# Kernel optimization log

Measured on AMD Instinct MI355X. Metric: run time of the kernel, lower is better.

## Reference

```python
import jax, jax.numpy as jnp
import numpy as np

HID, INP, BATCH, TIME = 1024, 512, 128, 256


def _kaiming(key, d1, d2, gain):
    # kaiming_normal_: std = gain / sqrt(fan_in), fan_in = d2
    return jax.random.normal(key, (d1, d2), jnp.float32) * (gain / np.sqrt(d2))


def setup_inputs() -> dict:
    key = jax.random.key(0)
    ks = jax.random.split(key, 9)
    g_lin = 1.0          # nonlinearity='linear'
    g_tanh = 5.0 / 3.0   # nonlinearity='tanh'
    inp = {
        "x": jax.random.normal(ks[0], (BATCH, TIME, INP), jnp.float32),
        "c": jnp.zeros((HID, BATCH), jnp.float32),
        "h": jnp.zeros((HID, BATCH), jnp.float32),
        "W_gx": _kaiming(ks[1], HID, INP, g_lin),
        "W_ix": _kaiming(ks[2], HID, INP, g_lin),
        "W_fx": _kaiming(ks[3], HID, INP, g_lin),
        "W_ox": _kaiming(ks[4], HID, INP, g_lin),
        "W_gh": _kaiming(ks[5], HID, HID, g_tanh),
        "W_ih": _kaiming(ks[6], HID, HID, g_tanh),
        "W_fh": _kaiming(ks[7], HID, HID, g_tanh),
        "W_oh": _kaiming(ks[8], HID, HID, g_tanh),
        "b_g": jnp.zeros((HID, 1), jnp.float32),
        "b_i": jnp.zeros((HID, 1), jnp.float32),
        "b_f": jnp.zeros((HID, 1), jnp.float32),
        "b_o": jnp.zeros((HID, 1), jnp.float32),
    }
    return inp


def reference(x, c, h, W_gx, W_ix, W_fx, W_ox, W_gh, W_ih, W_fh, W_oh,
              b_g, b_i, b_f, b_o):
    Hd = W_gx.shape[0]
    # Fuse the four gate GEMMs into one: same math, single contraction.
    Wx = jnp.concatenate([W_gx, W_ix, W_fx, W_ox], axis=0)   # (4H, I)
    Wh = jnp.concatenate([W_gh, W_ih, W_fh, W_oh], axis=0)   # (4H, H)
    b = jnp.concatenate([b_g, b_i, b_f, b_o], axis=0)[:, 0]  # (4H,)
    # Precompute all input projections: (T, B, 4H)
    xs = jnp.einsum('bti,gi->tbg', x, Wx)

    def step(carry, xt):
        c_t, h_t = carry                      # (B, H)
        z = xt + h_t @ Wh.T + b               # (B, 4H)
        g = jnp.tanh(z[:, :Hd])
        i = jax.nn.sigmoid(z[:, Hd:2 * Hd])
        f = jax.nn.sigmoid(z[:, 2 * Hd:3 * Hd])
        o = jax.nn.sigmoid(z[:, 3 * Hd:])
        c_n = g * i + c_t * f
        h_n = jnp.tanh(c_n) * o
        return (c_n, h_n), None

    (c_f, h_f), _ = jax.lax.scan(step, (c.T, h.T), xs)
    return h_f.T  # (H, B), matching the torch layout
```

## Files before the change

### kernel.cpp

```cpp
#include <hip/hip_runtime.h>
#include <cstdint>
#include <cstddef>

#define HID 1024
#define INP 512
#define BATCH 128
#define TSTEPS 256
#define NK16 96
#define ZSLOTS 32

using short8  = __attribute__((ext_vector_type(8))) short;
using f32x16  = __attribute__((ext_vector_type(16))) float;

#define LD8(p) (*(const short8*)(p))
#define MFMA32(a,b,c) __builtin_amdgcn_mfma_f32_32x32x16_bf16((a),(b),(c),0,0,0)

static __device__ __forceinline__ unsigned short f2bf(float f) {
    union { float f; unsigned int u; } v; v.f = f;
    unsigned int r = v.u + 0x7fffu + ((v.u >> 16) & 1u);
    return (unsigned short)(r >> 16);
}
static __device__ __forceinline__ float bf2f(unsigned short b) {
    union { unsigned int u; float f; } v; v.u = ((unsigned int)b) << 16;
    return v.f;
}
static __device__ __forceinline__ float sigmoid_f(float z) {
    return 1.0f / (1.0f + __expf(-z));
}
static __device__ __forceinline__ float tanh_f(float z) {
    return 2.0f / (1.0f + __expf(-2.0f * z)) - 1.0f;
}


__global__ void prep_w(const float* __restrict__ Wgx, const float* __restrict__ Wix,
                       const float* __restrict__ Wfx, const float* __restrict__ Wox,
                       const float* __restrict__ Wgh, const float* __restrict__ Wih,
                       const float* __restrict__ Wfh, const float* __restrict__ Woh,
                       unsigned short* __restrict__ wfrag)
{
    const int k16 = blockIdx.x;
    const int s   = blockIdx.y;
    const int tid  = threadIdx.x;
    const int lane = tid >> 2;
    const int e0   = (tid & 3) * 2;
    const int row  = s * 32 + (lane & 31);
    const int k    = k16 * 16 + (lane >> 5) * 8 + e0;
    const int j = row >> 2;
    const int g = row & 3;
    float f0, f1;
    if (k < INP) {
        const float* wx = (g == 0 ? Wgx : g == 1 ? Wix : g == 2 ? Wfx : Wox) + (size_t)j * INP;
        f0 = wx[k]; f1 = wx[k + 1];
    } else {
        const float* wh = (g == 0 ? Wgh : g == 1 ? Wih : g == 2 ? Wfh : Woh) + (size_t)j * HID;
        f0 = wh[k - INP]; f1 = wh[k - INP + 1];
    }
    ushort2 hi, lo;
    hi.x = f2bf(f0); lo.x = f2bf(f0 - bf2f(hi.x));
    hi.y = f2bf(f1); lo.y = f2bf(f1 - bf2f(hi.y));
    unsigned short* base = wfrag + ((size_t)(s * NK16 + k16) * 2) * 512 + lane * 8 + e0;
    *(ushort2*)(base)       = hi;
    *(ushort2*)(base + 512) = lo;
}

__global__ void prep_x(const float* __restrict__ x, unsigned short* __restrict__ xfrag)
{
    const int k16x = blockIdx.x;
    const int t    = blockIdx.y;
    const int tid  = threadIdx.x;
    const int cg   = tid >> 6;
    const int lane = tid & 63;
    const int col  = cg * 32 + (lane & 31);
    const int k0   = k16x * 16 + (lane >> 5) * 8;
    const float* src = x + ((size_t)col * TSTEPS + t) * INP + k0;
    const float4 v0 = *(const float4*)(src);
    const float4 v1 = *(const float4*)(src + 4);
    ushort4 h0, l0, h1, l1;
    h0.x = f2bf(v0.x); l0.x = f2bf(v0.x - bf2f(h0.x));
    h0.y = f2bf(v0.y); l0.y = f2bf(v0.y - bf2f(h0.y));
    h0.z = f2bf(v0.z); l0.z = f2bf(v0.z - bf2f(h0.z));
    h0.w = f2bf(v0.w); l0.w = f2bf(v0.w - bf2f(h0.w));
    h1.x = f2bf(v1.x); l1.x = f2bf(v1.x - bf2f(h1.x));
    h1.y = f2bf(v1.y); l1.y = f2bf(v1.y - bf2f(h1.y));
    h1.z = f2bf(v1.z); l1.z = f2bf(v1.z - bf2f(h1.z));
    h1.w = f2bf(v1.w); l1.w = f2bf(v1.w - bf2f(h1.w));
    unsigned short* base = xfrag +
        ((size_t)(((size_t)t * 32 + k16x) * 4 + cg) * 2) * 512 + lane * 8;
    *(ushort4*)(base)           = h0;
    *(ushort4*)(base + 4)       = h1;
    *(ushort4*)(base + 512)     = l0;
    *(ushort4*)(base + 512 + 4) = l1;
}

__global__ void prep_state(const float* __restrict__ cin, const float* __restrict__ hin,
                           float* __restrict__ cdst, unsigned short* __restrict__ hfrag0)
{
    const int idx = blockIdx.x * 256 + threadIdx.x;
    cdst[idx] = cin[idx];
    const int j = idx >> 7;
    const int b = idx & 127;
    float f = hin[idx];
    unsigned short hh = f2bf(f);
    unsigned short hl = f2bf(f - bf2f(hh));
    const int k16h = j >> 4;
    const int hlf  = (j >> 3) & 1;
    const int e    = j & 7;
    const int cg   = b >> 5;
    const int lane = 32 * hlf + (b & 31);
    unsigned short* base = hfrag0 +
        ((size_t)((k16h * 4 + cg) * 2) * 512) + lane * 8 + e;
    base[0]   = hh;
    base[512] = hl;
}

__global__ __launch_bounds__(512, 2) void gemm_z0(
    const unsigned short* __restrict__ wfrag,
    const unsigned short* __restrict__ xfrag,
    float* __restrict__ z0,
    const float* __restrict__ bg, const float* __restrict__ bi,
    const float* __restrict__ bf_, const float* __restrict__ bo,
    int tbase)
{
    const int tid  = threadIdx.x;
    const int wv   = tid >> 6;
    const int lane = tid & 63;
    const int l31  = lane & 31;
    const int hl   = lane >> 5;
    const int cw   = wv & 1;
    const int kq   = wv >> 1;
    const int s    = blockIdx.x;
    const int t    = tbase + blockIdx.y;
    const int tslot = t & (ZSLOTS - 1);

    const unsigned short* pA = wfrag + ((size_t)(s * NK16 + kq) * 2) * 512 + lane * 8;
    const unsigned short* pB = xfrag + (size_t)t * 131072
                             + (size_t)(4 * kq + 2 * cw) * 1024 + lane * 8;

    f32x16 a0A, a0B, a1A, a1B;
#pragma unroll
    for (int r = 0; r < 16; ++r) { a0A[r]=0.f; a0B[r]=0.f; a1A[r]=0.f; a1B[r]=0.f; }

#pragma unroll
    for (int m = 0; m < 8; ++m) {
        short8 Ah  = LD8(pA);
        short8 Al  = LD8(pA + 512);
        short8 B0h = LD8(pB);
        short8 B0l = LD8(pB + 512);
        short8 B1h = LD8(pB + 1024);
        short8 B1l = LD8(pB + 1536);
        pA += 4096; pB += 16384;
        a0A = MFMA32(Ah, B0h, a0A);
        a1A = MFMA32(Ah, B1h, a1A);
        a0B = MFMA32(Ah, B0l, a0B);
        a1B = MFMA32(Ah, B1l, a1B);
        a0A = MFMA32(Al, B0h, a0A);
        a1A = MFMA32(Al, B1h, a1A);
    }

    __shared__ float part[2][32][128];

    if (kq >= 2) {
#pragma unroll
        for (int r = 0; r < 16; ++r) {
            const int lr = (r & 3) + 8 * (r >> 2) + 4 * hl;
            part[kq - 2][lr][(2 * cw)     * 32 + l31] = a0A[r] + a0B[r];
            part[kq - 2][lr][(2 * cw + 1) * 32 + l31] = a1A[r] + a1B[r];
        }
    }
    __syncthreads();
    if (kq < 2) {
#pragma unroll
        for (int r = 0; r < 16; ++r) {
            const int lr = (r & 3) + 8 * (r >> 2) + 4 * hl;
            part[kq][lr][(2 * cw)     * 32 + l31] += a0A[r] + a0B[r];
            part[kq][lr][(2 * cw + 1) * 32 + l31] += a1A[r] + a1B[r];
        }
    }
    __syncthreads();

    {
        const int lr = tid >> 4;
        const int c0 = (tid & 15) * 8;
        const int g  = lr & 3;
        const int j  = s * 8 + (lr >> 2);
        const float bb = (g == 0 ? bg : g == 1 ? bi : g == 2 ? bf_ : bo)[j];
        float z[8];
#pragma unroll
        for (int cc = 0; cc < 8; ++cc)
            z[cc] = part[0][lr][c0 + cc] + part[1][lr][c0 + cc] + bb;
        float* dst = z0 + (((size_t)tslot * 128 + s) * 32 + lr) * 128 + c0;
        *(float4*)(dst)     = make_float4(z[0], z[1], z[2], z[3]);
        *(float4*)(dst + 4) = make_float4(z[4], z[5], z[6], z[7]);
    }
}

__global__ __launch_bounds__(512, 1) void lstm_step(
    const unsigned short* __restrict__ wfrag,
    const unsigned short* __restrict__ xfrag,
    const float* __restrict__ z0,
    const unsigned short* __restrict__ hin,
    unsigned short* __restrict__ hout,
    float* __restrict__ cst,
    const float* __restrict__ bg, const float* __restrict__ bi,
    const float* __restrict__ bf_, const float* __restrict__ bo,
    float* __restrict__ outf, int t)
{
    const int tid  = threadIdx.x;
    const int wv   = tid >> 6;
    const int lane = tid & 63;
    const int l31  = lane & 31;
    const int hl   = lane >> 5;
    const int bx   = blockIdx.x;

    const int xcd     = bx & 7;
    const int ii      = bx >> 3;
    const int s       = xcd * 16 + (ii >> 1);
    const int cb      = ii & 1;
    const int colbase = cb << 6;
    const int J0      = s * 8;

    const int ejl  = tid >> 6;
    const int ecl  = tid & 63;
    const int ej   = J0 + ejl;
    const int ecol = colbase + ecl;

    float add0, add1, add2, add3;
    if (z0) {
        const float* zp = z0 + (((size_t)(t & (ZSLOTS - 1)) * 128 + s) * 32
                                + 4 * ejl) * 128 + ecol;
        add0 = zp[0]; add1 = zp[128]; add2 = zp[256]; add3 = zp[384];
    } else {
        add0 = bg[ej]; add1 = bi[ej]; add2 = bf_[ej]; add3 = bo[ej];
    }
    const size_t ci = (size_t)ej * BATCH + ecol;
    float cold = cst[ci];

    f32x16 a0A, a0B, a1A, a1B;
#pragma unroll
    for (int r = 0; r < 16; ++r) { a0A[r]=0.f; a0B[r]=0.f; a1A[r]=0.f; a1B[r]=0.f; }

    const size_t bOff = (size_t)(4 * wv + 2 * cb) * 1024 + lane * 8;

    if (z0) {
        const unsigned short* pA = wfrag + ((size_t)(s * NK16 + 32 + wv) * 2) * 512 + lane * 8;
        const unsigned short* pH = hin + bOff;
#pragma unroll
        for (int m = 0; m < 8; ++m) {
            short8 Ah  = LD8(pA);
            short8 Al  = LD8(pA + 512);
            short8 B0h = LD8(pH);
            short8 B0l = LD8(pH + 512);
            short8 B1h = LD8(pH + 1024);
            short8 B1l = LD8(pH + 1536);
            pA += 8192; pH += 32768;
            a0A = MFMA32(Ah, B0h, a0A);
            a1A = MFMA32(Ah, B1h, a1A);
            a0B = MFMA32(Ah, B0l, a0B);
            a1B = MFMA32(Ah, B1l, a1B);
            a0A = MFMA32(Al, B0h, a0A);
            a1A = MFMA32(Al, B1h, a1A);
        }
    } else {
        const unsigned short* pA = wfrag + ((size_t)(s * NK16 + wv) * 2) * 512 + lane * 8;
        const unsigned short* pX = xfrag + (size_t)t * 131072 + bOff;
#pragma unroll
        for (int m = 0; m < 4; ++m) {
            short8 Ah  = LD8(pA);
            short8 Al  = LD8(pA + 512);
            short8 B0h = LD8(pX);
            short8 B0l = LD8(pX + 512);
            short8 B1h = LD8(pX + 1024);
            short8 B1l = LD8(pX + 1536);
            pA += 8192; pX += 32768;
            a0A = MFMA32(Ah, B0h, a0A);
            a1A = MFMA32(Ah, B1h, a1A);
            a0B = MFMA32(Ah, B0l, a0B);
            a1B = MFMA32(Ah, B1l, a1B);
            a0A = MFMA32(Al, B0h, a0A);
            a1A = MFMA32(Al, B1h, a1A);
        }
        const unsigned short* pH = hin + bOff;
#pragma unroll
        for (int m = 0; m < 8; ++m) {
            short8 Ah  = LD8(pA);
            short8 Al  = LD8(pA + 512);
            short8 B0h = LD8(pH);
            short8 B0l = LD8(pH + 512);
            short8 B1h = LD8(pH + 1024);
            short8 B1l = LD8(pH + 1536);
            pA += 8192; pH += 32768;
            a0A = MFMA32(Ah, B0h, a0A);
            a1A = MFMA32(Ah, B1h, a1A);
            a0B = MFMA32(Ah, B0l, a0B);
            a1B = MFMA32(Ah, B1l, a1B);
            a0A = MFMA32(Al, B0h, a0A);
            a1A = MFMA32(Al, B1h, a1A);
        }
    }

    __shared__ float part[8][32][64];
#pragma unroll
    for (int r = 0; r < 16; ++r) {
        const int lr = (r & 3) + 8 * (r >> 2) + 4 * hl;
        part[wv][lr][l31]      = a0A[r] + a0B[r];
        part[wv][lr][32 + l31] = a1A[r] + a1B[r];
    }
    __syncthreads();

    {
        const int r0 = 4 * ejl;
        float z0g = add0, z1g = add1, z2g = add2, z3g = add3;
#pragma unroll
        for (int p = 0; p < 8; ++p) {
            z0g += part[p][r0 + 0][ecl];
            z1g += part[p][r0 + 1][ecl];
            z2g += part[p][r0 + 2][ecl];
            z3g += part[p][r0 + 3][ecl];
        }
        float gg = tanh_f(z0g);
        float ig = sigmoid_f(z1g);
        float fg = sigmoid_f(z2g);
        float og = sigmoid_f(z3g);
        float cn = gg * ig + cold * fg;
        cst[ci] = cn;
        float hh = tanh_f(cn) * og;
        unsigned short hb  = f2bf(hh);
        unsigned short hlo = f2bf(hh - bf2f(hb));
        const int k16h  = s >> 1;
        const int cgg   = (colbase >> 5) + (ecl >> 5);
        const int lane8 = 32 * (s & 1) + (ecl & 31);
        unsigned short* dst = hout +
            ((size_t)((k16h * 4 + cgg) * 2) * 512) + lane8 * 8 + ejl;
        dst[0]   = hb;
        dst[512] = hlo;
        if (outf) outf[ci] = hh;
    }
}

extern "C" void kernel_launch(void* const* d_in, const int* in_sizes, int n_in,
                              void* d_out, int out_size, void* d_ws, size_t ws_size,
                              hipStream_t stream)
{
    const float* x   = (const float*)d_in[0];
    const float* c0v = (const float*)d_in[1];
    const float* h0v = (const float*)d_in[2];
    const float* Wgx = (const float*)d_in[3];
    const float* Wix = (const float*)d_in[4];
    const float* Wfx = (const float*)d_in[5];
    const float* Wox = (const float*)d_in[6];
    const float* Wgh = (const float*)d_in[7];
    const float* Wih = (const float*)d_in[8];
    const float* Wfh = (const float*)d_in[9];
    const float* Woh = (const float*)d_in[10];
    const float* bg  = (const float*)d_in[11];
    const float* bi  = (const float*)d_in[12];
    const float* bf  = (const float*)d_in[13];
    const float* bo  = (const float*)d_in[14];

    unsigned short* wfrag = (unsigned short*)d_ws;
    unsigned short* xfrag = wfrag + (size_t)128 * NK16 * 2 * 512;
    unsigned short* hf0   = xfrag + (size_t)TSTEPS * 32 * 4 * 2 * 512;
    unsigned short* hf1   = hf0 + (size_t)64 * 4 * 2 * 512;
    float* cst            = (float*)(hf1 + (size_t)64 * 4 * 2 * 512);
    float* z0             = (float*)(cst + (size_t)HID * BATCH);

    const size_t needA = (size_t)((char*)(z0 + (size_t)ZSLOTS * 4096 * 128) - (char*)d_ws);
    const bool useA = (ws_size >= needA);

    unsigned short* hf[2] = { hf0, hf1 };
    float* outp = (float*)d_out;

    prep_w<<<dim3(NK16, 128), dim3(256), 0, stream>>>(Wgx, Wix, Wfx, Wox,
                                                      Wgh, Wih, Wfh, Woh, wfrag);
    prep_x<<<dim3(32, TSTEPS), dim3(256), 0, stream>>>(x, xfrag);
    prep_state<<<dim3(512), dim3(256), 0, stream>>>(c0v, h0v, cst, hf[0]);

    if (useA) {
        for (int q = 0; q < TSTEPS / ZSLOTS; ++q) {
            gemm_z0<<<dim3(128, ZSLOTS), dim3(512), 0, stream>>>(
                wfrag, xfrag, z0, bg, bi, bf, bo, q * ZSLOTS);
            for (int tt = 0; tt < ZSLOTS; ++tt) {
                const int t = q * ZSLOTS + tt;
                lstm_step<<<dim3(256), dim3(512), 0, stream>>>(
                    wfrag, xfrag, z0, hf[t & 1], hf[(t + 1) & 1],
                    cst, bg, bi, bf, bo,
                    (t == TSTEPS - 1) ? outp : nullptr, t);
            }
        }
    } else {
        for (int t = 0; t < TSTEPS; ++t) {
            lstm_step<<<dim3(256), dim3(512), 0, stream>>>(
                wfrag, xfrag, nullptr, hf[t & 1], hf[(t + 1) & 1],
                cst, bg, bi, bf, bo,
                (t == TSTEPS - 1) ? outp : nullptr, t);
        }
    }
}
```

Before: 2.514 ms.

## Replace per-step LSTM launches with a persistent cooperative kernel using flag barriers

Replaces the 256 per-timestep lstm_step launches and the batched input-projection GEMM with a single cooperative persistent kernel. Each block keeps its cell state in registers and computes both the x and h projections each step. Blocks synchronise through per-block atomic step flags in global memory, and h is written into a 32-slot ring buffer. This removes kernel launch overhead and the z0 round trip through memory. The cost is spin-wait polling on flags and a dependence on all 256 blocks being co-resident, which relies on relaxed atomics with an occasional acquire fence.

```diff
diff --git a/kernel.cpp b/kernel.cpp
--- a/kernel.cpp
+++ b/kernel.cpp
@@ -7,7 +7,9 @@
 #define BATCH 128
 #define TSTEPS 256
 #define NK16 96
-#define ZSLOTS 32
+#define HSLOTS 32
+#define NBLK_CHUNK 256
+#define HSLOT ((size_t)64 * 4 * 2 * 512)
 
 using short8  = __attribute__((ext_vector_type(8))) short;
 using f32x16  = __attribute__((ext_vector_type(16))) float;
@@ -93,8 +95,10 @@
 }
 
 __global__ void prep_state(const float* __restrict__ cin, const float* __restrict__ hin,
-                           float* __restrict__ cdst, unsigned short* __restrict__ hfrag0)
-{
+                           float* __restrict__ cdst, unsigned short* __restrict__ hslot,
+                           unsigned* __restrict__ flags)
+{
+    if (blockIdx.x == 0) flags[threadIdx.x] = 0u;
     const int idx = blockIdx.x * 256 + threadIdx.x;
     cdst[idx] = cin[idx];
     const int j = idx >> 7;
@@ -107,97 +111,178 @@
     const int e    = j & 7;
     const int cg   = b >> 5;
     const int lane = 32 * hlf + (b & 31);
-    unsigned short* base = hfrag0 +
+    unsigned short* base = hslot +
         ((size_t)((k16h * 4 + cg) * 2) * 512) + lane * 8 + e;
     base[0]   = hh;
     base[512] = hl;
 }
 
-__global__ __launch_bounds__(512, 2) void gemm_z0(
+__global__ __launch_bounds__(512, 1) void lstm_persist(
     const unsigned short* __restrict__ wfrag,
     const unsigned short* __restrict__ xfrag,
-    float* __restrict__ z0,
+    unsigned short* __restrict__ hbuf,
+    float* __restrict__ cst,
     const float* __restrict__ bg, const float* __restrict__ bi,
     const float* __restrict__ bf_, const float* __restrict__ bo,
-    int tbase)
+    float* __restrict__ outf,
+    unsigned* __restrict__ flags)
 {
     const int tid  = threadIdx.x;
     const int wv   = tid >> 6;
     const int lane = tid & 63;
     const int l31  = lane & 31;
     const int hl   = lane >> 5;
-    const int cw   = wv & 1;
-    const int kq   = wv >> 1;
-    const int s    = blockIdx.x;
-    const int t    = tbase + blockIdx.y;
-    const int tslot = t & (ZSLOTS - 1);
-
-    const unsigned short* pA = wfrag + ((size_t)(s * NK16 + kq) * 2) * 512 + lane * 8;
-    const unsigned short* pB = xfrag + (size_t)t * 131072
-                             + (size_t)(4 * kq + 2 * cw) * 1024 + lane * 8;
-
-    f32x16 a0A, a0B, a1A, a1B;
-#pragma unroll
-    for (int r = 0; r < 16; ++r) { a0A[r]=0.f; a0B[r]=0.f; a1A[r]=0.f; a1B[r]=0.f; }
-
-#pragma unroll
-    for (int m = 0; m < 8; ++m) {
-        short8 Ah  = LD8(pA);
-        short8 Al  = LD8(pA + 512);
-        short8 B0h = LD8(pB);
-        short8 B0l = LD8(pB + 512);
-        short8 B1h = LD8(pB + 1024);
-        short8 B1l = LD8(pB + 1536);
-        pA += 4096; pB += 16384;
-        a0A = MFMA32(Ah, B0h, a0A);
-        a1A = MFMA32(Ah, B1h, a1A);
-        a0B = MFMA32(Ah, B0l, a0B);
-        a1B = MFMA32(Ah, B1l, a1B);
-        a0A = MFMA32(Al, B0h, a0A);
-        a1A = MFMA32(Al, B1h, a1A);
-    }
-
-    __shared__ float part[2][32][128];
-
-    if (kq >= 2) {
+    const int bx   = blockIdx.x;
+
+    const int xcd     = bx & 7;
+    const int ii      = bx >> 3;
+    const int s       = xcd * 16 + (ii >> 1);
+    const int cb      = ii & 1;
+    const int colbase = cb << 6;
+
+    const int ejl  = tid >> 6;
+    const int ecl  = tid & 63;
+    const int ej   = s * 8 + ejl;
+    const int ecol = colbase + ecl;
+    const size_t ci = (size_t)ej * BATCH + ecol;
+
+    const float bias0 = bg[ej], bias1 = bi[ej], bias2 = bf_[ej], bias3 = bo[ej];
+    float creg = cst[ci];
+
+    const size_t bOff = (size_t)(4 * wv + 2 * cb) * 1024 + lane * 8;
+    const int k16h = s >> 1;
+
+    const unsigned short* pAx0 = wfrag + ((size_t)(s * NK16 + wv) * 2) * 512 + lane * 8;
+    const unsigned short* pAh0 = wfrag + ((size_t)(s * NK16 + 32 + wv) * 2) * 512 + lane * 8;
+
+    __shared__ float part[8][32][64];
+    __shared__ unsigned long long hstage[256];
+    unsigned short* hs16 = (unsigned short*)hstage;
+
+#pragma unroll 1
+    for (int t = 0; t < TSTEPS; ++t) {
+        f32x16 a0A, a0B, a1A, a1B;
+#pragma unroll
+        for (int r = 0; r < 16; ++r) { a0A[r]=0.f; a0B[r]=0.f; a1A[r]=0.f; a1B[r]=0.f; }
+
+        {
+            const unsigned short* pA = pAx0;
+            const unsigned short* pX = xfrag + (size_t)t * 131072 + bOff;
+#pragma unroll
+            for (int m = 0; m < 4; ++m) {
+                short8 Ah  = LD8(pA);
+                short8 Al  = LD8(pA + 512);
+                short8 B0h = LD8(pX);
+                short8 B0l = LD8(pX + 512);
+                short8 B1h = LD8(pX + 1024);
+                short8 B1l = LD8(pX + 1536);
+                pA += 8192; pX += 32768;
+                a0A = MFMA32(Ah, B0h, a0A);
+                a1A = MFMA32(Ah, B1h, a1A);
+                a0B = MFMA32(Ah, B0l, a0B);
+                a1B = MFMA32(Ah, B1l, a1B);
+                a0A = MFMA32(Al, B0h, a0A);
+                a1A = MFMA32(Al, B1h, a1A);
+            }
+        }
+
+        if (t > 0) {
+            const unsigned target = (unsigned)t;
+            int done;
+            int guard = 0;
+            do {
+                unsigned v = target;
+                if (tid < 256)
+                    v = __hip_atomic_load(&flags[tid], __ATOMIC_RELAXED,
+                                          __HIP_MEMORY_SCOPE_AGENT);
+                done = __syncthreads_count(v >= target);
+                if (done < 512) __builtin_amdgcn_s_sleep(1);
+            } while (done < 512 && ++guard < (1 << 20));
+            asm volatile("" ::: "memory");
+            __builtin_amdgcn_sched_barrier(0);
+            if ((t & 31) == 0)
+                __builtin_amdgcn_fence(__ATOMIC_ACQUIRE, "agent");
+        }
+
+        {
+            const unsigned short* pA = pAh0;
+            const unsigned short* pH = hbuf + (size_t)((t + HSLOTS - 1) & (HSLOTS - 1)) * HSLOT + bOff;
+#pragma unroll
+            for (int m = 0; m < 8; ++m) {
+                short8 Ah  = LD8(pA);
+                short8 Al  = LD8(pA + 512);
+                short8 B0h = LD8(pH);
+                short8 B0l = LD8(pH + 512);
+                short8 B1h = LD8(pH + 1024);
+                short8 B1l = LD8(pH + 1536);
+                pA += 8192; pH += 32768;
+                a0A = MFMA32(Ah, B0h, a0A);
+                a1A = MFMA32(Ah, B1h, a1A);
+                a0B = MFMA32(Ah, B0l, a0B);
+                a1B = MFMA32(Ah, B1l, a1B);
+                a0A = MFMA32(Al, B0h, a0A);
+                a1A = MFMA32(Al, B1h, a1A);
+            }
+        }
+
 #pragma unroll
         for (int r = 0; r < 16; ++r) {
             const int lr = (r & 3) + 8 * (r >> 2) + 4 * hl;
-            part[kq - 2][lr][(2 * cw)     * 32 + l31] = a0A[r] + a0B[r];
-            part[kq - 2][lr][(2 * cw + 1) * 32 + l31] = a1A[r] + a1B[r];
-        }
-    }
-    __syncthreads();
-    if (kq < 2) {
-#pragma unroll
-        for (int r = 0; r < 16; ++r) {
-            const int lr = (r & 3) + 8 * (r >> 2) + 4 * hl;
-            part[kq][lr][(2 * cw)     * 32 + l31] += a0A[r] + a0B[r];
-            part[kq][lr][(2 * cw + 1) * 32 + l31] += a1A[r] + a1B[r];
-        }
-    }
-    __syncthreads();
-
-    {
-        const int lr = tid >> 4;
-        const int c0 = (tid & 15) * 8;
-        const int g  = lr & 3;
-        const int j  = s * 8 + (lr >> 2);
-        const float bb = (g == 0 ? bg : g == 1 ? bi : g == 2 ? bf_ : bo)[j];
-        float z[8];
-#pragma unroll
-        for (int cc = 0; cc < 8; ++cc)
-            z[cc] = part[0][lr][c0 + cc] + part[1][lr][c0 + cc] + bb;
-        float* dst = z0 + (((size_t)tslot * 128 + s) * 32 + lr) * 128 + c0;
-        *(float4*)(dst)     = make_float4(z[0], z[1], z[2], z[3]);
-        *(float4*)(dst + 4) = make_float4(z[4], z[5], z[6], z[7]);
-    }
+            part[wv][lr][l31]      = a0A[r] + a0B[r];
+            part[wv][lr][32 + l31] = a1A[r] + a1B[r];
+        }
+        __syncthreads();
+
+        {
+            const int r0 = 4 * ejl;
+            float z0g = bias0, z1g = bias1, z2g = bias2, z3g = bias3;
+#pragma unroll
+            for (int p = 0; p < 8; ++p) {
+                z0g += part[p][r0 + 0][ecl];
+                z1g += part[p][r0 + 1][ecl];
+                z2g += part[p][r0 + 2][ecl];
+                z3g += part[p][r0 + 3][ecl];
+            }
+            float gg = tanh_f(z0g);
+            float ig = sigmoid_f(z1g);
+            float fg = sigmoid_f(z2g);
+            float og = sigmoid_f(z3g);
+            float cn = gg * ig + creg * fg;
+            creg = cn;
+            float hh = tanh_f(cn) * og;
+            unsigned short hb  = f2bf(hh);
+            unsigned short hlo = f2bf(hh - bf2f(hb));
+            hs16[((ecl >> 5) * 2 + 0) * 256 + (ecl & 31) * 8 + ejl] = hb;
+            hs16[((ecl >> 5) * 2 + 1) * 256 + (ecl & 31) * 8 + ejl] = hlo;
+            if (outf && t == TSTEPS - 1) outf[ci] = hh;
+        }
+        __syncthreads();
+
+        {
+            unsigned short* hout = hbuf + (size_t)(t & (HSLOTS - 1)) * HSLOT;
+            if (tid < 256) {
+                const int r   = tid >> 6;
+                const int w   = tid & 63;
+                const int cgg = 2 * cb + (r >> 1);
+                const int p   = r & 1;
+                const size_t uo = ((size_t)((k16h * 4 + cgg) * 2 + p)) * 512
+                                + 32 * (s & 1) * 8 + w * 4;
+                __hip_atomic_store((unsigned long long*)(hout + uo), hstage[tid],
+                                   __ATOMIC_RELAXED, __HIP_MEMORY_SCOPE_AGENT);
+            }
+        }
+        asm volatile("s_waitcnt vmcnt(0)" ::: "memory");
+        __syncthreads();
+        if (tid == 0)
+            __hip_atomic_store(&flags[bx], (unsigned)(t + 1),
+                               __ATOMIC_RELAXED, __HIP_MEMORY_SCOPE_AGENT);
+    }
+    cst[ci] = creg;
 }
 
 __global__ __launch_bounds__(512, 1) void lstm_step(
     const unsigned short* __restrict__ wfrag,
     const unsigned short* __restrict__ xfrag,
-    const float* __restrict__ z0,
     const unsigned short* __restrict__ hin,
     unsigned short* __restrict__ hout,
     float* __restrict__ cst,
@@ -217,21 +302,13 @@
     const int s       = xcd * 16 + (ii >> 1);
     const int cb      = ii & 1;
     const int colbase = cb << 6;
-    const int J0      = s * 8;
 
     const int ejl  = tid >> 6;
     const int ecl  = tid & 63;
-    const int ej   = J0 + ejl;
+    const int ej   = s * 8 + ejl;
     const int ecol = colbase + ecl;
 
-    float add0, add1, add2, add3;
-    if (z0) {
-        const float* zp = z0 + (((size_t)(t & (ZSLOTS - 1)) * 128 + s) * 32
-                                + 4 * ejl) * 128 + ecol;
-        add0 = zp[0]; add1 = zp[128]; add2 = zp[256]; add3 = zp[384];
-    } else {
-        add0 = bg[ej]; add1 = bi[ej]; add2 = bf_[ej]; add3 = bo[ej];
-    }
+    float add0 = bg[ej], add1 = bi[ej], add2 = bf_[ej], add3 = bo[ej];
     const size_t ci = (size_t)ej * BATCH + ecol;
     float cold = cst[ci];
 
@@ -241,26 +318,7 @@
 
     const size_t bOff = (size_t)(4 * wv + 2 * cb) * 1024 + lane * 8;
 
-    if (z0) {
-        const unsigned short* pA = wfrag + ((size_t)(s * NK16 + 32 + wv) * 2) * 512 + lane * 8;
-        const unsigned short* pH = hin + bOff;
-#pragma unroll
-        for (int m = 0; m < 8; ++m) {
-            short8 Ah  = LD8(pA);
-            short8 Al  = LD8(pA + 512);
-            short8 B0h = LD8(pH);
-            short8 B0l = LD8(pH + 512);
-            short8 B1h = LD8(pH + 1024);
-            short8 B1l = LD8(pH + 1536);
-            pA += 8192; pH += 32768;
-            a0A = MFMA32(Ah, B0h, a0A);
-            a1A = MFMA32(Ah, B1h, a1A);
-            a0B = MFMA32(Ah, B0l, a0B);
-            a1B = MFMA32(Ah, B1l, a1B);
-            a0A = MFMA32(Al, B0h, a0A);
-            a1A = MFMA32(Al, B1h, a1A);
-        }
-    } else {
+    {
         const unsigned short* pA = wfrag + ((size_t)(s * NK16 + wv) * 2) * 512 + lane * 8;
         const unsigned short* pX = xfrag + (size_t)t * 131072 + bOff;
 #pragma unroll
@@ -359,38 +417,50 @@
 
     unsigned short* wfrag = (unsigned short*)d_ws;
     unsigned short* xfrag = wfrag + (size_t)128 * NK16 * 2 * 512;
-    unsigned short* hf0   = xfrag + (size_t)TSTEPS * 32 * 4 * 2 * 512;
-    unsigned short* hf1   = hf0 + (size_t)64 * 4 * 2 * 512;
-    float* cst            = (float*)(hf1 + (size_t)64 * 4 * 2 * 512);
-    float* z0             = (float*)(cst + (size_t)HID * BATCH);
-
-    const size_t needA = (size_t)((char*)(z0 + (size_t)ZSLOTS * 4096 * 128) - (char*)d_ws);
+    unsigned short* hbuf  = xfrag + (size_t)TSTEPS * 32 * 4 * 2 * 512;
+    float* cst            = (float*)(hbuf + (size_t)HSLOTS * HSLOT);
+    unsigned* flags       = (unsigned*)(cst + (size_t)HID * BATCH);
+
+    const size_t needA = (size_t)((char*)(flags + 1024) - (char*)d_ws);
     const bool useA = (ws_size >= needA);
 
-    unsigned short* hf[2] = { hf0, hf1 };
     float* outp = (float*)d_out;
 
     prep_w<<<dim3(NK16, 128), dim3(256), 0, stream>>>(Wgx, Wix, Wfx, Wox,
                                                       Wgh, Wih, Wfh, Woh, wfrag);
     prep_x<<<dim3(32, TSTEPS), dim3(256), 0, stream>>>(x, xfrag);
-    prep_state<<<dim3(512), dim3(256), 0, stream>>>(c0v, h0v, cst, hf[0]);
-
+    prep_state<<<dim3(512), dim3(256), 0, stream>>>(c0v, h0v, cst,
+                                                    hbuf + (size_t)(HSLOTS - 1) * HSLOT,
+                                                    flags);
+
+    bool done = false;
     if (useA) {
-        for (int q = 0; q < TSTEPS / ZSLOTS; ++q) {
-            gemm_z0<<<dim3(128, ZSLOTS), dim3(512), 0, stream>>>(
-                wfrag, xfrag, z0, bg, bi, bf, bo, q * ZSLOTS);
-            for (int tt = 0; tt < ZSLOTS; ++tt) {
-                const int t = q * ZSLOTS + tt;
-                lstm_step<<<dim3(256), dim3(512), 0, stream>>>(
-                    wfrag, xfrag, z0, hf[t & 1], hf[(t + 1) & 1],
-                    cst, bg, bi, bf, bo,
-                    (t == TSTEPS - 1) ? outp : nullptr, t);
-            }
-        }
-    } else {
+        const unsigned short* a_wfrag = wfrag;
+        const unsigned short* a_xfrag = xfrag;
+        unsigned short* a_hbuf = hbuf;
+        float* a_cst = cst;
+        const float* a_bg = bg; const float* a_bi = bi;
+        const float* a_bf = bf; const float* a_bo = bo;
+        float* a_out = outp;
+        unsigned* a_flags = flags;
+        void* kargs[] = { (void*)&a_wfrag, (void*)&a_xfrag, (void*)&a_hbuf,
+                          (void*)&a_cst, (void*)&a_bg, (void*)&a_bi,
+                          (void*)&a_bf, (void*)&a_bo, (void*)&a_out,
+                          (void*)&a_flags };
+        hipError_t ce = hipLaunchCooperativeKernel(
+            (const void*)lstm_persist, dim3(NBLK_CHUNK), dim3(512),
+            kargs, 0, stream);
+        done = (ce == hipSuccess);
+    }
+
+    if (!done) {
+        unsigned short* hfA = hbuf + (size_t)(HSLOTS - 1) * HSLOT;
+        unsigned short* hfB = hbuf + (size_t)(HSLOTS - 2) * HSLOT;
         for (int t = 0; t < TSTEPS; ++t) {
+            const unsigned short* hin = (t & 1) ? hfB : hfA;
+            unsigned short* hout      = (t & 1) ? hfA : hfB;
             lstm_step<<<dim3(256), dim3(512), 0, stream>>>(
-                wfrag, xfrag, nullptr, hf[t & 1], hf[(t + 1) & 1],
+                wfrag, xfrag, hin, hout,
                 cst, bg, bi, bf, bo,
                 (t == TSTEPS - 1) ? outp : nullptr, t);
         }
```

Result: faster. 2.297 ms (-8.6%).
